# Kernel tuning notes

Measured on AMD Instinct MI355X. Metric: run time of the kernel, lower is better.

Reference implementation:

```python
import jax, jax.numpy as jnp
import numpy as np

NUM_HEADS = 12


def _rel_indices(H, W):
    # [N, N, 3] with channels (dx, dy, dx^2+dy^2), N = H*W
    indx = jnp.arange(W)[None, :] - jnp.arange(W)[:, None]          # [W, W]
    indx = jnp.tile(indx, (H, H))                                    # [N, N]
    indy = jnp.arange(H)[None, :] - jnp.arange(H)[:, None]          # [H, H]
    indy = jnp.repeat(jnp.repeat(indy, W, axis=0), W, axis=1)        # [N, N]
    indd = indx ** 2 + indy ** 2
    return jnp.stack([indx, indy, indd], axis=-1).astype(jnp.float32)


def setup_inputs() -> dict:
    key = jax.random.key(0)
    ks = jax.random.split(key, 8)
    B, N, C = 16, 576, 768
    std = 0.02
    return {
        "x": jax.random.normal(ks[0], (B, N, C), dtype=jnp.float32),
        "Wq": jax.random.normal(ks[1], (C, C), dtype=jnp.float32) * std,
        "Wk": jax.random.normal(ks[2], (C, C), dtype=jnp.float32) * std,
        "Wv": jax.random.normal(ks[3], (C, C), dtype=jnp.float32) * std,
        "Wproj": jax.random.normal(ks[4], (C, C), dtype=jnp.float32) * std,
        "bproj": jnp.zeros((C,), dtype=jnp.float32),
        "pos_w": jax.random.normal(ks[5], (3, NUM_HEADS), dtype=jnp.float32) * std,
        "pos_b": jnp.zeros((NUM_HEADS,), dtype=jnp.float32),
        "gating": jnp.ones((NUM_HEADS,), dtype=jnp.float32),
        "H": 24,
        "W": 24,
    }


def reference(x, Wq, Wk, Wv, Wproj, bproj, pos_w, pos_b, gating, H, W):
    B, N, C = x.shape
    h = gating.shape[0]
    d = C // h
    scale = d ** (-0.5)

    def heads(t):  # [B,N,C] -> [B,h,N,d]
        return t.reshape(B, N, h, d).transpose(0, 2, 1, 3)

    q = heads(x @ Wq)
    k = heads(x @ Wk)
    v = heads(x @ Wv)

    # content scores: [B,h,N,N]
    patch_score = jax.nn.softmax(jnp.einsum('bhnd,bhmd->bhnm', q, k) * scale, axis=-1)

    # positional scores: shared across batch, [h,N,N]
    rel = _rel_indices(H, W)                      # [N,N,3]
    pos_score = jnp.einsum('nmc,ch->hnm', rel, pos_w) + pos_b[:, None, None]
    pos_score = jax.nn.softmax(pos_score, axis=-1)

    gate = jax.nn.sigmoid(gating)[None, :, None, None]  # [1,h,1,1]
    attn = (1.0 - gate) * patch_score + gate * pos_score[None]
    attn = attn / jnp.sum(attn, axis=-1, keepdims=True)

    out = jnp.einsum('bhnm,bhmd->bhnd', attn, v)         # [B,h,N,d]
    out = out.transpose(0, 2, 1, 3).reshape(B, N, C)
    return out @ Wproj + bproj
```

## Files before the change

kernel.cpp:

```cpp
#include <hip/hip_runtime.h>
#include <math.h>

#define B_ 16
#define N_ 576
#define C_ 768
#define NH 12
#define D_ 64
#define STR 68
#define QKV 2304

typedef unsigned short u16;
typedef __bf16 bf16x8 __attribute__((ext_vector_type(8)));
typedef float f32x4 __attribute__((ext_vector_type(4)));

__device__ __forceinline__ u16 f2bf(float f) {
    unsigned u = __builtin_bit_cast(unsigned, f);
    unsigned r = (u + 0x7FFFu + ((u >> 16) & 1u)) >> 16;
    return (u16)r;
}

__device__ __forceinline__ bf16x8 ldsF8u(const u16* p) {
    union { uint2 u[2]; bf16x8 v; } t;
    t.u[0] = *(const uint2*)p;
    t.u[1] = *(const uint2*)(p + 4);
    return t.v;
}
__device__ __forceinline__ bf16x8 ldsF8a(const u16* p) {
    union { uint4 u; bf16x8 v; } t;
    t.u = *(const uint4*)p;
    return t.v;
}

__device__ __forceinline__ void gload16(const u16* g, u16* l) {
    __builtin_amdgcn_global_load_lds(
        (const __attribute__((address_space(1))) void*)g,
        (__attribute__((address_space(3))) void*)l,
        16, 0, 0);
}

__global__ __launch_bounds__(256)
void conv_x_kernel(const float* __restrict__ x, u16* __restrict__ xb)
{
    int i = blockIdx.x * 256 + threadIdx.x;
    float4 v = ((const float4*)x)[i];
    u16 o[4] = {f2bf(v.x), f2bf(v.y), f2bf(v.z), f2bf(v.w)};
    *(uint2*)&xb[(size_t)i * 4] = *(const uint2*)o;
}

__global__ __launch_bounds__(256)
void transpose_w_kernel(const float* __restrict__ src, u16* __restrict__ dst)
{
    __shared__ float t[32][33];
    const int bx = blockIdx.x * 32, by = blockIdx.y * 32;
    const int tx = threadIdx.x & 31, ty = threadIdx.x >> 5;
#pragma unroll
    for (int i = 0; i < 32; i += 8)
        t[ty + i][tx] = src[(size_t)(by + ty + i) * C_ + bx + tx];
    __syncthreads();
#pragma unroll
    for (int i = 0; i < 32; i += 8)
        dst[(size_t)(bx + ty + i) * C_ + by + tx] = f2bf(t[tx][ty + i]);
}

__global__ __launch_bounds__(256)
void transpose_v_kernel(const u16* __restrict__ qkvb, u16* __restrict__ vtb)
{
    __shared__ u16 t[64 * 72];
    const int n0 = blockIdx.x * 64;
    const int bh = blockIdx.y;
    const int b = bh / NH, h = bh % NH;
    const int tid = threadIdx.x;
    const u16* src = qkvb + ((size_t)b * N_ + n0) * QKV + 2 * C_ + h * D_;
#pragma unroll
    for (int p = 0; p < 2; ++p) {
        int idx = p * 256 + tid;
        int r = idx >> 3, c = (idx & 7) << 3;
        *(uint4*)&t[r * 72 + c] = *(const uint4*)(src + (size_t)r * QKV + c);
    }
    __syncthreads();
    u16* dst = vtb + (size_t)bh * D_ * N_ + n0;
#pragma unroll
    for (int p = 0; p < 2; ++p) {
        int idx = p * 256 + tid;
        int dd = idx >> 3, n8 = (idx & 7) << 3;
        u16 o[8];
#pragma unroll
        for (int j = 0; j < 8; ++j) o[j] = t[(n8 + j) * 72 + dd];
        *(uint4*)(dst + (size_t)dd * N_ + n8) = *(const uint4*)o;
    }
}

__global__ __launch_bounds__(256)
void mfma_gemm(const u16* __restrict__ A,
               const u16* __restrict__ BT,
               const float* __restrict__ bias,
               float* __restrict__ out,
               u16* __restrict__ outb,
               int ldo, int mode)
{
    const int K = C_;
    __shared__ __align__(16) u16 As[128 * 64];
    __shared__ __align__(16) u16 Bs[128 * 64];
    const int tid = threadIdx.x;
    const int wave = tid >> 6, lane = tid & 63;
    const int quad = lane >> 4, l16 = lane & 15;
    const int wy = wave >> 1, wx = wave & 1;

    const int gx = gridDim.x;
    const int nwg = gx * gridDim.y;
    int o = blockIdx.y * gx + blockIdx.x;
    o = (o & 7) * (nwg >> 3) + (o >> 3);
    const int tm = (o / gx) * 128, tn = (o % gx) * 128;

    const int lr = lane >> 3;
    const int sc = ((lane & 7) ^ lr) * 8;

    f32x4 acc[4][4];
#pragma unroll
    for (int i = 0; i < 4; ++i)
#pragma unroll
        for (int j = 0; j < 4; ++j)
            acc[i][j] = (f32x4){0.f, 0.f, 0.f, 0.f};

    for (int k0 = 0; k0 < K; k0 += 64) {
        __syncthreads();
#pragma unroll
        for (int t = 0; t < 4; ++t) {
            const int rg = wave * 32 + t * 8;
            gload16(A  + (size_t)(tm + rg + lr) * K + k0 + sc, &As[rg * 64]);
            gload16(BT + (size_t)(tn + rg + lr) * K + k0 + sc, &Bs[rg * 64]);
        }
        __syncthreads();

#pragma unroll
        for (int kh = 0; kh < 2; ++kh) {
            bf16x8 aA[4], bB[4];
#pragma unroll
            for (int i = 0; i < 4; ++i) {
                const int s = (kh * 4 + quad) ^ (l16 & 7);
                aA[i] = ldsF8a(&As[(wy * 64 + i * 16 + l16) * 64 + s * 8]);
            }
#pragma unroll
            for (int j = 0; j < 4; ++j) {
                const int s = (kh * 4 + quad) ^ (l16 & 7);
                bB[j] = ldsF8a(&Bs[(wx * 64 + j * 16 + l16) * 64 + s * 8]);
            }
#pragma unroll
            for (int i = 0; i < 4; ++i)
#pragma unroll
                for (int j = 0; j < 4; ++j)
                    acc[i][j] = __builtin_amdgcn_mfma_f32_16x16x32_bf16(aA[i], bB[j], acc[i][j], 0, 0, 0);
        }
    }

    if (mode == 0) {
#pragma unroll
        for (int i = 0; i < 4; ++i) {
#pragma unroll
            for (int r = 0; r < 4; ++r) {
                const int m = tm + wy * 64 + i * 16 + quad * 4 + r;
#pragma unroll
                for (int j = 0; j < 4; ++j) {
                    const int c = tn + wx * 64 + j * 16 + l16;
                    out[(size_t)m * ldo + c] = acc[i][j][r] + bias[c];
                }
            }
        }
    } else {
        const float scale = (tn < C_) ? 0.125f : 1.0f;
#pragma unroll
        for (int i = 0; i < 4; ++i) {
#pragma unroll
            for (int r = 0; r < 4; ++r) {
                const int m = tm + wy * 64 + i * 16 + quad * 4 + r;
#pragma unroll
                for (int j = 0; j < 4; ++j) {
                    const int c = tn + wx * 64 + j * 16 + l16;
                    outb[(size_t)m * ldo + c] = f2bf(acc[i][j][r] * scale);
                }
            }
        }
    }
}

__global__ __launch_bounds__(256)
void pos_softmax_kernel(const float* __restrict__ pos_w,
                        const float* __restrict__ pos_b,
                        const int* __restrict__ Hp,
                        const int* __restrict__ Wp,
                        u16* __restrict__ pos_out)
{
    const int n = blockIdx.x;
    const int hh = blockIdx.y;
    const int tid = threadIdx.x;
    __shared__ float srow[N_];
    __shared__ float wred[4];
    const int Ww = Wp[0];
    (void)Hp;
    const float w0 = pos_w[0 * NH + hh];
    const float w1 = pos_w[1 * NH + hh];
    const float w2 = pos_w[2 * NH + hh];
    const float bb = pos_b[hh];
    const int nx = n % Ww, ny = n / Ww;

    float lmax = -1e30f;
    for (int m = tid; m < N_; m += 256) {
        float dx = (float)((m % Ww) - nx);
        float dy = (float)((m / Ww) - ny);
        float sc = dx * w0 + dy * w1 + (dx * dx + dy * dy) * w2 + bb;
        srow[m] = sc;
        lmax = fmaxf(lmax, sc);
    }
#pragma unroll
    for (int off = 32; off; off >>= 1) lmax = fmaxf(lmax, __shfl_down(lmax, off, 64));
    if ((tid & 63) == 0) wred[tid >> 6] = lmax;
    __syncthreads();
    float M = fmaxf(fmaxf(wred[0], wred[1]), fmaxf(wred[2], wred[3]));
    __syncthreads();

    float lsum = 0.f;
    for (int m = tid; m < N_; m += 256) {
        float e = __expf(srow[m] - M);
        srow[m] = e;
        lsum += e;
    }
#pragma unroll
    for (int off = 32; off; off >>= 1) lsum += __shfl_down(lsum, off, 64);
    if ((tid & 63) == 0) wred[tid >> 6] = lsum;
    __syncthreads();
    float inv = 1.0f / (wred[0] + wred[1] + wred[2] + wred[3]);

    u16* op = pos_out + ((size_t)hh * N_ + n) * N_;
    for (int m = tid; m < N_; m += 256) op[m] = f2bf(srow[m] * inv);
}

__global__ __launch_bounds__(256)
void attn_kernel(const u16* __restrict__ qkvb,
                 const u16* __restrict__ vt,
                 const u16* __restrict__ pos,
                 const float* __restrict__ gating,
                 u16* __restrict__ ao)
{
    const int gx = gridDim.x;
    const int nwg = gx * gridDim.y;
    int o = blockIdx.y * gx + blockIdx.x;
    o = (o & 7) * (nwg >> 3) + (o >> 3);
    const int qt = o % gx;
    const int yb = o / gx;
    const int h = yb >> 4, b = yb & 15;
    const int tid = threadIdx.x;
    const int wave = tid >> 6, lane = tid & 63;
    const int quad = lane >> 4, l16 = lane & 15;

    __shared__ u16 smem[4 * 64 * STR];
    u16* Kt = smem;
    u16* Vs = smem + 64 * STR;
    u16* Pp = smem + 2 * 64 * STR;
    u16* Pb = smem + 3 * 64 * STR;

    const u16* qptr  = qkvb + ((size_t)b * N_ + qt * 64) * QKV + h * D_;
    const u16* kbase = qkvb + (size_t)b * N_ * QKV + C_ + h * D_;
    const u16* vbase = vt + (size_t)(b * NH + h) * D_ * N_;
    const u16* pbase = pos + ((size_t)h * N_ + qt * 64) * N_;

    const int sr = tid >> 3;
    const int scol = (tid & 7) << 3;

#pragma unroll
    for (int p = 0; p < 2; ++p) {
        int r = p * 32 + sr;
        uint4 d = *(const uint4*)(qptr + (size_t)r * QKV + scol);
        *(uint2*)&Pb[r * STR + scol]     = make_uint2(d.x, d.y);
        *(uint2*)&Pb[r * STR + scol + 4] = make_uint2(d.z, d.w);
    }
    __syncthreads();

    const int arow = wave * 16 + l16;
    bf16x8 aq0 = ldsF8u(&Pb[arow * STR + quad * 8]);
    bf16x8 aq1 = ldsF8u(&Pb[arow * STR + 32 + quad * 8]);

    uint4 rk[2], rv[2], rp[2];
    auto loadT = [&](int m0) {
#pragma unroll
        for (int p = 0; p < 2; ++p) {
            int r = p * 32 + sr;
            rk[p] = *(const uint4*)(kbase + (size_t)(m0 + r) * QKV + scol);
            rv[p] = *(const uint4*)(vbase + (size_t)r * N_ + m0 + scol);
            rp[p] = *(const uint4*)(pbase + (size_t)r * N_ + m0 + scol);
        }
    };
    auto writeT = [&]() {
#pragma unroll
        for (int p = 0; p < 2; ++p) {
            int r = p * 32 + sr;
            *(uint2*)&Kt[r * STR + scol]     = make_uint2(rk[p].x, rk[p].y);
            *(uint2*)&Kt[r * STR + scol + 4] = make_uint2(rk[p].z, rk[p].w);
            *(uint2*)&Vs[r * STR + scol]     = make_uint2(rv[p].x, rv[p].y);
            *(uint2*)&Vs[r * STR + scol + 4] = make_uint2(rv[p].z, rv[p].w);
            *(uint2*)&Pp[r * STR + scol]     = make_uint2(rp[p].x, rp[p].y);
            *(uint2*)&Pp[r * STR + scol + 4] = make_uint2(rp[p].z, rp[p].w);
        }
    };

    loadT(0);

    f32x4 oc[4], op[4];
#pragma unroll
    for (int nt = 0; nt < 4; ++nt) {
        oc[nt] = (f32x4){0.f, 0.f, 0.f, 0.f};
        op[nt] = (f32x4){0.f, 0.f, 0.f, 0.f};
    }
    float lrun[4] = {0.f, 0.f, 0.f, 0.f};

    for (int mt = 0; mt < 9; ++mt) {
        __syncthreads();
        writeT();
        __syncthreads();
        if (mt < 8) loadT((mt + 1) * 64);

        f32x4 s[4];
#pragma unroll
        for (int nt = 0; nt < 4; ++nt) {
            bf16x8 b0 = ldsF8u(&Kt[(nt * 16 + l16) * STR + quad * 8]);
            bf16x8 b1 = ldsF8u(&Kt[(nt * 16 + l16) * STR + 32 + quad * 8]);
            f32x4 z = (f32x4){0.f, 0.f, 0.f, 0.f};
            z = __builtin_amdgcn_mfma_f32_16x16x32_bf16(aq0, b0, z, 0, 0, 0);
            z = __builtin_amdgcn_mfma_f32_16x16x32_bf16(aq1, b1, z, 0, 0, 0);
            s[nt] = z;
        }

#pragma unroll
        for (int r = 0; r < 4; ++r) {
            const int prow = (wave * 16 + quad * 4 + r) * STR;
            float e0 = __expf(s[0][r]);
            float e1 = __expf(s[1][r]);
            float e2 = __expf(s[2][r]);
            float e3 = __expf(s[3][r]);
            Pb[prow +  0 + l16] = f2bf(e0);
            Pb[prow + 16 + l16] = f2bf(e1);
            Pb[prow + 32 + l16] = f2bf(e2);
            Pb[prow + 48 + l16] = f2bf(e3);
            lrun[r] += (e0 + e1) + (e2 + e3);
        }
        asm volatile("s_waitcnt lgkmcnt(0)" ::: "memory");

#pragma unroll
        for (int ks = 0; ks < 2; ++ks) {
            bf16x8 ap   = ldsF8u(&Pb[arow * STR + ks * 32 + quad * 8]);
            bf16x8 apos = ldsF8u(&Pp[arow * STR + ks * 32 + quad * 8]);
#pragma unroll
            for (int nt = 0; nt < 4; ++nt) {
                bf16x8 bv = ldsF8u(&Vs[(nt * 16 + l16) * STR + ks * 32 + quad * 8]);
                oc[nt] = __builtin_amdgcn_mfma_f32_16x16x32_bf16(ap,   bv, oc[nt], 0, 0, 0);
                op[nt] = __builtin_amdgcn_mfma_f32_16x16x32_bf16(apos, bv, op[nt], 0, 0, 0);
            }
        }
    }

#pragma unroll
    for (int r = 0; r < 4; ++r) {
        lrun[r] += __shfl_xor(lrun[r], 1, 64);
        lrun[r] += __shfl_xor(lrun[r], 2, 64);
        lrun[r] += __shfl_xor(lrun[r], 4, 64);
        lrun[r] += __shfl_xor(lrun[r], 8, 64);
    }

    const float g = 1.f / (1.f + __expf(-gating[h]));
#pragma unroll
    for (int r = 0; r < 4; ++r) {
        const float sc = (1.f - g) / lrun[r];
        const int row = qt * 64 + wave * 16 + quad * 4 + r;
#pragma unroll
        for (int nt = 0; nt < 4; ++nt) {
            ao[((size_t)b * N_ + row) * C_ + h * D_ + nt * 16 + l16] =
                f2bf(oc[nt][r] * sc + g * op[nt][r]);
        }
    }
}

extern "C" void kernel_launch(void* const* d_in, const int* in_sizes, int n_in,
                              void* d_out, int out_size, void* d_ws, size_t ws_size,
                              hipStream_t stream)
{
    const float* x      = (const float*)d_in[0];
    const float* Wq     = (const float*)d_in[1];
    const float* Wk     = (const float*)d_in[2];
    const float* Wv     = (const float*)d_in[3];
    const float* Wproj  = (const float*)d_in[4];
    const float* bproj  = (const float*)d_in[5];
    const float* pos_w  = (const float*)d_in[6];
    const float* pos_b  = (const float*)d_in[7];
    const float* gating = (const float*)d_in[8];
    const int*   Hp     = (const int*)d_in[9];
    const int*   Wp     = (const int*)d_in[10];
    float* out = (float*)d_out;

    const size_t xe = (size_t)B_ * N_ * C_;
    const size_t we = (size_t)C_ * C_;
    const size_t qe = (size_t)B_ * N_ * QKV;
    const size_t pe = (size_t)NH * N_ * N_;
    u16* xb   = (u16*)d_ws;
    u16* wt   = xb + xe;
    u16* wtp  = wt + 3 * we;
    u16* qkvb = wtp + we;
    u16* vtb  = qkvb + qe;
    u16* posb = vtb + xe;
    u16* aob  = posb + pe;
    size_t need = (size_t)(3 * xe + 4 * we + qe + pe) * sizeof(u16);
    if (ws_size < need) return;

    conv_x_kernel<<<dim3((unsigned)(xe / 1024)), 256, 0, stream>>>(x, xb);
    dim3 tgrid(24, 24);
    transpose_w_kernel<<<tgrid, 256, 0, stream>>>(Wq, wt);
    transpose_w_kernel<<<tgrid, 256, 0, stream>>>(Wk, wt + we);
    transpose_w_kernel<<<tgrid, 256, 0, stream>>>(Wv, wt + 2 * we);
    transpose_w_kernel<<<tgrid, 256, 0, stream>>>(Wproj, wtp);

    mfma_gemm<<<dim3(18, 72), 256, 0, stream>>>(xb, wt, nullptr, nullptr,
                                                qkvb, QKV, 1);
    transpose_v_kernel<<<dim3(9, B_ * NH), 256, 0, stream>>>(qkvb, vtb);
    pos_softmax_kernel<<<dim3(N_, NH), 256, 0, stream>>>(pos_w, pos_b, Hp, Wp, posb);
    attn_kernel<<<dim3(9, NH * B_), 256, 0, stream>>>(qkvb, vtb, posb, gating, aob);
    mfma_gemm<<<dim3(6, 72), 256, 0, stream>>>(aob, wtp, bproj, out,
                                               nullptr, C_, 0);
}
```

Before: 240.3 us.

## Fuse positional softmax into attention kernel and compute scores on the fly

Drops the separate positional-softmax kernel and its materialized [heads,N,N] bf16 buffer. The attention kernel now computes the positional logits per element from a decomposed quadratic form (a per-column alpha table in shared memory plus per-row terms), exponentiates them, and accumulates the row sum for normalization at the end. This removes a kernel launch and the global reads of the pos tiles repeated across every batch, in exchange for extra exp and integer work inside the inner loop. The grid width is hard-coded to 24 and max-subtraction is replaced with a clamp, which limits generality and numerical robustness.

```diff
diff --git a/kernel.cpp b/kernel.cpp
--- a/kernel.cpp
+++ b/kernel.cpp
@@ -184,60 +184,10 @@
 }
 
 __global__ __launch_bounds__(256)
-void pos_softmax_kernel(const float* __restrict__ pos_w,
-                        const float* __restrict__ pos_b,
-                        const int* __restrict__ Hp,
-                        const int* __restrict__ Wp,
-                        u16* __restrict__ pos_out)
-{
-    const int n = blockIdx.x;
-    const int hh = blockIdx.y;
-    const int tid = threadIdx.x;
-    __shared__ float srow[N_];
-    __shared__ float wred[4];
-    const int Ww = Wp[0];
-    (void)Hp;
-    const float w0 = pos_w[0 * NH + hh];
-    const float w1 = pos_w[1 * NH + hh];
-    const float w2 = pos_w[2 * NH + hh];
-    const float bb = pos_b[hh];
-    const int nx = n % Ww, ny = n / Ww;
-
-    float lmax = -1e30f;
-    for (int m = tid; m < N_; m += 256) {
-        float dx = (float)((m % Ww) - nx);
-        float dy = (float)((m / Ww) - ny);
-        float sc = dx * w0 + dy * w1 + (dx * dx + dy * dy) * w2 + bb;
-        srow[m] = sc;
-        lmax = fmaxf(lmax, sc);
-    }
-#pragma unroll
-    for (int off = 32; off; off >>= 1) lmax = fmaxf(lmax, __shfl_down(lmax, off, 64));
-    if ((tid & 63) == 0) wred[tid >> 6] = lmax;
-    __syncthreads();
-    float M = fmaxf(fmaxf(wred[0], wred[1]), fmaxf(wred[2], wred[3]));
-    __syncthreads();
-
-    float lsum = 0.f;
-    for (int m = tid; m < N_; m += 256) {
-        float e = __expf(srow[m] - M);
-        srow[m] = e;
-        lsum += e;
-    }
-#pragma unroll
-    for (int off = 32; off; off >>= 1) lsum += __shfl_down(lsum, off, 64);
-    if ((tid & 63) == 0) wred[tid >> 6] = lsum;
-    __syncthreads();
-    float inv = 1.0f / (wred[0] + wred[1] + wred[2] + wred[3]);
-
-    u16* op = pos_out + ((size_t)hh * N_ + n) * N_;
-    for (int m = tid; m < N_; m += 256) op[m] = f2bf(srow[m] * inv);
-}
-
-__global__ __launch_bounds__(256)
 void attn_kernel(const u16* __restrict__ qkvb,
                  const u16* __restrict__ vt,
-                 const u16* __restrict__ pos,
+                 const float* __restrict__ pos_w,
+                 const float* __restrict__ pos_b,
                  const float* __restrict__ gating,
                  u16* __restrict__ ao)
 {
@@ -252,16 +202,27 @@
     const int wave = tid >> 6, lane = tid & 63;
     const int quad = lane >> 4, l16 = lane & 15;
 
-    __shared__ u16 smem[4 * 64 * STR];
+    __shared__ u16 smem[3 * 64 * STR];
+    __shared__ float alpha[N_];
     u16* Kt = smem;
     u16* Vs = smem + 64 * STR;
-    u16* Pp = smem + 2 * 64 * STR;
-    u16* Pb = smem + 3 * 64 * STR;
+    u16* Pb = smem + 2 * 64 * STR;
+
+    const float w0 = pos_w[0 * NH + h];
+    const float w1 = pos_w[1 * NH + h];
+    const float w2 = pos_w[2 * NH + h];
+    const float bb = pos_b[h];
+
+    for (int m = tid; m < N_; m += 256) {
+        int my = (m * 2731) >> 16;
+        int mx = m - my * 24;
+        float fx = (float)mx, fy = (float)my;
+        alpha[m] = fmaf(fx, w0, fmaf(fy, w1, (fx * fx + fy * fy) * w2));
+    }
 
     const u16* qptr  = qkvb + ((size_t)b * N_ + qt * 64) * QKV + h * D_;
     const u16* kbase = qkvb + (size_t)b * N_ * QKV + C_ + h * D_;
     const u16* vbase = vt + (size_t)(b * NH + h) * D_ * N_;
-    const u16* pbase = pos + ((size_t)h * N_ + qt * 64) * N_;
 
     const int sr = tid >> 3;
     const int scol = (tid & 7) << 3;
@@ -279,14 +240,22 @@
     bf16x8 aq0 = ldsF8u(&Pb[arow * STR + quad * 8]);
     bf16x8 aq1 = ldsF8u(&Pb[arow * STR + 32 + quad * 8]);
 
-    uint4 rk[2], rv[2], rp[2];
+    const int nrow = qt * 64 + arow;
+    const int nyi = (nrow * 2731) >> 16;
+    const int nxi = nrow - nyi * 24;
+    const float nxf = (float)nxi, nyf = (float)nyi;
+    const float beta = fmaf(nxf * nxf + nyf * nyf, w2,
+                            fmaf(-nxf, w0, fmaf(-nyf, w1, bb)));
+    const float gam = -2.f * w2 * nxf;
+    const float del = -2.f * w2 * nyf;
+
+    uint4 rk[2], rv[2];
     auto loadT = [&](int m0) {
 #pragma unroll
         for (int p = 0; p < 2; ++p) {
             int r = p * 32 + sr;
             rk[p] = *(const uint4*)(kbase + (size_t)(m0 + r) * QKV + scol);
             rv[p] = *(const uint4*)(vbase + (size_t)r * N_ + m0 + scol);
-            rp[p] = *(const uint4*)(pbase + (size_t)r * N_ + m0 + scol);
         }
     };
     auto writeT = [&]() {
@@ -297,8 +266,6 @@
             *(uint2*)&Kt[r * STR + scol + 4] = make_uint2(rk[p].z, rk[p].w);
             *(uint2*)&Vs[r * STR + scol]     = make_uint2(rv[p].x, rv[p].y);
             *(uint2*)&Vs[r * STR + scol + 4] = make_uint2(rv[p].z, rv[p].w);
-            *(uint2*)&Pp[r * STR + scol]     = make_uint2(rp[p].x, rp[p].y);
-            *(uint2*)&Pp[r * STR + scol + 4] = make_uint2(rp[p].z, rp[p].w);
         }
     };
 
@@ -311,6 +278,7 @@
         op[nt] = (f32x4){0.f, 0.f, 0.f, 0.f};
     }
     float lrun[4] = {0.f, 0.f, 0.f, 0.f};
+    float lpos = 0.f;
 
     for (int mt = 0; mt < 9; ++mt) {
         __syncthreads();
@@ -346,8 +314,20 @@
 
 #pragma unroll
         for (int ks = 0; ks < 2; ++ks) {
-            bf16x8 ap   = ldsF8u(&Pb[arow * STR + ks * 32 + quad * 8]);
-            bf16x8 apos = ldsF8u(&Pp[arow * STR + ks * 32 + quad * 8]);
+            bf16x8 ap = ldsF8u(&Pb[arow * STR + ks * 32 + quad * 8]);
+            bf16x8 apos;
+            const int mb = mt * 64 + ks * 32 + quad * 8;
+            const float* a8 = &alpha[mb];
+#pragma unroll
+            for (int e = 0; e < 8; ++e) {
+                int m = mb + e;
+                int my = (m * 2731) >> 16;
+                int mx = m - my * 24;
+                float s2 = fmaf((float)mx, gam, fmaf((float)my, del, beta)) + a8[e];
+                float ee = __expf(fminf(s2, 80.f));
+                lpos += ee;
+                apos[e] = (__bf16)ee;
+            }
 #pragma unroll
             for (int nt = 0; nt < 4; ++nt) {
                 bf16x8 bv = ldsF8u(&Vs[(nt * 16 + l16) * STR + ks * 32 + quad * 8]);
@@ -364,16 +344,20 @@
         lrun[r] += __shfl_xor(lrun[r], 4, 64);
         lrun[r] += __shfl_xor(lrun[r], 8, 64);
     }
+    lpos += __shfl_xor(lpos, 16, 64);
+    lpos += __shfl_xor(lpos, 32, 64);
 
     const float g = 1.f / (1.f + __expf(-gating[h]));
 #pragma unroll
     for (int r = 0; r < 4; ++r) {
         const float sc = (1.f - g) / lrun[r];
+        const float lp = __shfl(lpos, quad * 4 + r, 64);
+        const float scp = g / lp;
         const int row = qt * 64 + wave * 16 + quad * 4 + r;
 #pragma unroll
         for (int nt = 0; nt < 4; ++nt) {
             ao[((size_t)b * N_ + row) * C_ + h * D_ + nt * 16 + l16] =
-                f2bf(oc[nt][r] * sc + g * op[nt][r]);
+                f2bf(oc[nt][r] * sc + scp * op[nt][r]);
         }
     }
 }
@@ -391,22 +375,18 @@
     const float* pos_w  = (const float*)d_in[6];
     const float* pos_b  = (const float*)d_in[7];
     const float* gating = (const float*)d_in[8];
-    const int*   Hp     = (const int*)d_in[9];
-    const int*   Wp     = (const int*)d_in[10];
     float* out = (float*)d_out;
 
     const size_t xe = (size_t)B_ * N_ * C_;
     const size_t we = (size_t)C_ * C_;
     const size_t qe = (size_t)B_ * N_ * QKV;
-    const size_t pe = (size_t)NH * N_ * N_;
     u16* xb   = (u16*)d_ws;
     u16* wt   = xb + xe;
     u16* wtp  = wt + 3 * we;
     u16* qkvb = wtp + we;
     u16* vtb  = qkvb + qe;
-    u16* posb = vtb + xe;
-    u16* aob  = posb + pe;
-    size_t need = (size_t)(3 * xe + 4 * we + qe + pe) * sizeof(u16);
+    u16* aob  = vtb + xe;
+    size_t need = (size_t)(3 * xe + 4 * we + qe) * sizeof(u16);
     if (ws_size < need) return;
 
     conv_x_kernel<<<dim3((unsigned)(xe / 1024)), 256, 0, stream>>>(x, xb);
@@ -419,8 +399,8 @@
     mfma_gemm<<<dim3(18, 72), 256, 0, stream>>>(xb, wt, nullptr, nullptr,
                                                 qkvb, QKV, 1);
     transpose_v_kernel<<<dim3(9, B_ * NH), 256, 0, stream>>>(qkvb, vtb);
-    pos_softmax_kernel<<<dim3(N_, NH), 256, 0, stream>>>(pos_w, pos_b, Hp, Wp, posb);
-    attn_kernel<<<dim3(9, NH * B_), 256, 0, stream>>>(qkvb, vtb, posb, gating, aob);
+    attn_kernel<<<dim3(9, NH * B_), 256, 0, stream>>>(qkvb, vtb, pos_w, pos_b,
+                                                      gating, aob);
     mfma_gemm<<<dim3(6, 72), 256, 0, stream>>>(aob, wtp, bproj, out,
                                                nullptr, C_, 0);
 }
```

Result: no change. 245.1 us (+2.0%).
